# Kernel optimization log

Measured on AMD Instinct MI355X. Metric: run time of the kernel, lower is better.

## Reference

```python
import jax, jax.numpy as jnp
import numpy as np
from itertools import product

DEG = 3
N_COMPLEX = 8

def monomial_powers(deg: int, n_complex: int = 8) -> np.ndarray:
    out = [a for a in product(range(deg + 1), repeat=n_complex) if sum(a) <= deg]
    return np.asarray(out, dtype=np.int32)

POWERS = monomial_powers(DEG, N_COMPLEX)  # (K, 8)
K = POWERS.shape[0]                       # 165 for deg=3
MAXP = int(POWERS.max())                  # 3


def z_monomials(q):
    """q (B,16) real -> z^alpha (B,K) complex, z_k = q[:,k] + i q[:,k+8]."""
    x, y = q[:, :N_COMPLEX], q[:, N_COMPLEX:]
    z = jax.lax.complex(x, y)  # (B, 8)
    # power ladders z^0..z^MAXP : (B, 8, MAXP+1)
    cur = jnp.ones_like(z)
    ladders = [cur]
    for _ in range(MAXP):
        cur = cur * z
        ladders.append(cur)
    lad = jnp.stack(ladders, axis=-1)  # (B, 8, MAXP+1)
    mon = jnp.ones((q.shape[0], K), dtype=z.dtype)
    for c in range(N_COMPLEX):  # fixed 8 iterations (structural)
        mon = mon * lad[:, c, POWERS[:, c]]  # gather (B, K)
    return mon


def setup_inputs() -> dict:
    key = jax.random.key(0)
    kq, = jax.random.split(key, 1)
    B = 262144
    q = jax.random.normal(kq, (B, 16), dtype=jnp.float32)
    L_re = jnp.eye(K, dtype=jnp.float32)
    L_im = jnp.zeros((K, K), dtype=jnp.float32)
    return {"q": q, "L_re": L_re, "L_im": L_im}


def reference(q, L_re, L_im):
    # Cholesky-like factor L: strict lower triangles + softplus-positive diagonal
    Lr = jnp.tril(L_re, -1)
    Li = jnp.tril(L_im, -1)
    diag = jax.nn.softplus(jnp.diagonal(L_re)) + 0.001
    L = jax.lax.complex(Lr, Li) + jnp.diag(jax.lax.complex(diag, jnp.zeros_like(diag)))
    H = L @ L.conj().T                      # (K, K) Hermitian PSD
    z_a = z_monomials(q)                    # (B, K) complex64
    Hs = z_a @ H.T                          # (B, K)
    quad = jnp.sum(Hs * jnp.conj(z_a), axis=-1).real  # (B,)
    return jnp.log(quad + 1e-12)
```

## Files before the change

kernel.cpp:

```cpp
#include <hip/hip_runtime.h>
#include <hip/hip_bf16.h>
#include <utility>

#define DEV static __device__ __forceinline__

typedef __attribute__((ext_vector_type(8))) short bf16x8;
typedef __attribute__((ext_vector_type(4))) float f32x4;

constexpr int KM   = 165;
constexpr int IT   = 11;
constexpr int ITP  = 12;
constexpr int KS   = 6;
constexpr int NB   = ITP * KS * 64;
constexpr int ROWS = 64;

struct Pw { unsigned char p[8]; };
struct PwTab { Pw a[KM]; };
constexpr PwTab gen_powers() {
  PwTab t{};
  int idx = 0;
  for (int a0 = 0; a0 <= 3; ++a0)
  for (int a1 = 0; a1 <= 3-a0; ++a1)
  for (int a2 = 0; a2 <= 3-a0-a1; ++a2)
  for (int a3 = 0; a3 <= 3-a0-a1-a2; ++a3)
  for (int a4 = 0; a4 <= 3-a0-a1-a2-a3; ++a4)
  for (int a5 = 0; a5 <= 3-a0-a1-a2-a3-a4; ++a5)
  for (int a6 = 0; a6 <= 3-a0-a1-a2-a3-a4-a5; ++a6)
  for (int a7 = 0; a7 <= 3-a0-a1-a2-a3-a4-a5-a6; ++a7) {
    t.a[idx].p[0] = (unsigned char)a0; t.a[idx].p[1] = (unsigned char)a1;
    t.a[idx].p[2] = (unsigned char)a2; t.a[idx].p[3] = (unsigned char)a3;
    t.a[idx].p[4] = (unsigned char)a4; t.a[idx].p[5] = (unsigned char)a5;
    t.a[idx].p[6] = (unsigned char)a6; t.a[idx].p[7] = (unsigned char)a7;
    ++idx;
  }
  return t;
}
constexpr PwTab PW = gen_powers();

DEV unsigned int f2bf(float f) {
  unsigned int u = __builtin_bit_cast(unsigned int, f);
  u += 0x7fffu + ((u >> 16) & 1u);
  return u >> 16;
}
DEV unsigned int pack2(float lo, float hi) { return f2bf(lo) | (f2bf(hi) << 16); }
DEV float softplusf(float x) { return (x > 20.f) ? x : log1pf(expf(x)); }

template<int JJ, int C>
DEV void mono_step(float& r, float& i,
                   const float (&lx)[8][3], const float (&ly)[8][3]) {
  constexpr int pc = PW.a[JJ].p[C];
  if constexpr (pc > 0) {
    const float ar = lx[C][pc-1], ai = ly[C][pc-1];
    const float tr = r*ar - i*ai;
    i = r*ai + i*ar;
    r = tr;
  }
}
template<int JJ>
DEV void mono_eval(float& mr, float& mi,
                   const float (&lx)[8][3], const float (&ly)[8][3]) {
  float r = 1.f, i = 0.f;
  mono_step<JJ,0>(r,i,lx,ly); mono_step<JJ,1>(r,i,lx,ly);
  mono_step<JJ,2>(r,i,lx,ly); mono_step<JJ,3>(r,i,lx,ly);
  mono_step<JJ,4>(r,i,lx,ly); mono_step<JJ,5>(r,i,lx,ly);
  mono_step<JJ,6>(r,i,lx,ly); mono_step<JJ,7>(r,i,lx,ly);
  mr = r; mi = i;
}
template<int JJ>
DEV void mono_eval_guard(float& r, float& i,
                         const float (&lx)[8][3], const float (&ly)[8][3]) {
  if constexpr (JJ < KM) mono_eval<JJ>(r, i, lx, ly);
  else { r = 0.f; i = 0.f; }
}

template<int T, int... Us>
DEV void gen8(std::integer_sequence<int, Us...>, float (&mr)[8], float (&mi)[8],
              const float (&lx)[8][3], const float (&ly)[8][3]) {
  (mono_eval_guard<8*T + Us>(mr[Us], mi[Us], lx, ly), ...);
}
template<int T>
DEV void gen_chunk(const float (&lx)[8][3], const float (&ly)[8][3],
                   unsigned int* Xf, unsigned int* Yf, int mf, int r15) {
  constexpr int ksv = T >> 2;
  constexpr int gv  = T & 3;
  float mr[8], mi[8];
  gen8<T>(std::make_integer_sequence<int, 8>{}, mr, mi, lx, ly);
  uint4 ux, uy;
  ux.x = pack2(mr[0], mr[1]); ux.y = pack2(mr[2], mr[3]);
  ux.z = pack2(mr[4], mr[5]); ux.w = pack2(mr[6], mr[7]);
  uy.x = pack2(mi[0], mi[1]); uy.y = pack2(mi[2], mi[3]);
  uy.z = pack2(mi[4], mi[5]); uy.w = pack2(mi[6], mi[7]);
  const unsigned int off = (unsigned int)((mf*6 + ksv)*256 + gv*64 + r15*4);
  *(uint4*)&Xf[off] = ux;
  *(uint4*)&Yf[off] = uy;
}
template<int W, int... Ts>
DEV void gen_seq(std::integer_sequence<int, Ts...>,
                 const float (&lx)[8][3], const float (&ly)[8][3],
                 unsigned int* Xf, unsigned int* Yf, int mf, int r15) {
  (gen_chunk<6*W + Ts>(lx, ly, Xf, Yf, mf, r15), ...);
}
template<int W>
DEV void gen_wave(const float (&lx)[8][3], const float (&ly)[8][3],
                  unsigned int* Xf, unsigned int* Yf, int mf, int r15) {
  gen_seq<W>(std::make_integer_sequence<int, 6>{}, lx, ly, Xf, Yf, mf, r15);
}

__global__ void __launch_bounds__(256) poskahler_prep(
    const float* __restrict__ Lre, const float* __restrict__ Lim,
    uint4* __restrict__ bp, uint4* __restrict__ bq) {
  const int tid = blockIdx.x * 256 + threadIdx.x;
  if (tid >= NB) return;
  const int lane = tid & 63;
  const int it = (tid >> 6) / KS;
  const int ks = (tid >> 6) % KS;
  const int j  = it * 16 + (lane & 15);
  const int ib = ks * 32 + ((lane >> 4) << 3);
  float pr[8], qr[8];
#pragma unroll
  for (int e = 0; e < 8; ++e) { pr[e] = 0.f; qr[e] = 0.f; }
  if (j < KM) {
#pragma unroll
    for (int e = 0; e < 8; ++e) {
      const int i = ib + e;
      if (i < KM) {
        if (i > j)      { pr[e] = Lre[i*KM + j]; qr[e] = -Lim[i*KM + j]; }
        else if (i == j){ pr[e] = softplusf(Lre[j*KM + j]) + 0.001f; }
      }
    }
  }
  uint4 up, uq;
  up.x = pack2(pr[0], pr[1]); up.y = pack2(pr[2], pr[3]);
  up.z = pack2(pr[4], pr[5]); up.w = pack2(pr[6], pr[7]);
  uq.x = pack2(qr[0], qr[1]); uq.y = pack2(qr[2], qr[3]);
  uq.z = pack2(qr[4], qr[5]); uq.w = pack2(qr[6], qr[7]);
  bp[tid] = up;
  bq[tid] = uq;
}

template<int KSv>
DEV void load_tiles(const uint4* __restrict__ bp, const uint4* __restrict__ bq,
                    int wv, int lane, uint4 (&tp)[3], uint4 (&tq)[3]) {
#pragma unroll
  for (int ii = 0; ii < 3; ++ii) {
    const int it = 4*ii + wv;
    if (it <= 2*KSv + 1 && it < IT) {
      const int fs = (it*KS + KSv)*64 + lane;
      tp[ii] = bp[fs];
      tq[ii] = bq[fs];
    }
  }
}

template<int KSv>
DEV void compute_ks(const unsigned int* Xf, const unsigned int* Yf,
                    int wv, int lane,
                    const uint4 (&tp)[3], const uint4 (&tq)[3],
                    float (&aRe)[3][4][4], float (&aIm)[3][4][4]) {
  bf16x8 xf[4], yf[4];
#pragma unroll
  for (int mf = 0; mf < 4; ++mf) {
    const unsigned int off = (unsigned int)((mf*6 + KSv)*256 + lane*4);
    xf[mf] = __builtin_bit_cast(bf16x8, *(const uint4*)&Xf[off]);
    yf[mf] = __builtin_bit_cast(bf16x8, *(const uint4*)&Yf[off]);
  }
#pragma unroll
  for (int ii = 0; ii < 3; ++ii) {
    const int it = 4*ii + wv;
    if (it <= 2*KSv + 1 && it < IT) {
      const uint4 up = tp[ii];
      const uint4 uq = tq[ii];
      uint4 un;
      un.x = uq.x ^ 0x80008000u; un.y = uq.y ^ 0x80008000u;
      un.z = uq.z ^ 0x80008000u; un.w = uq.w ^ 0x80008000u;
      const bf16x8 vp = __builtin_bit_cast(bf16x8, up);
      const bf16x8 vq = __builtin_bit_cast(bf16x8, uq);
      const bf16x8 vn = __builtin_bit_cast(bf16x8, un);
#pragma unroll
      for (int mf = 0; mf < 4; ++mf) {
        f32x4 cre = { aRe[ii][mf][0], aRe[ii][mf][1], aRe[ii][mf][2], aRe[ii][mf][3] };
        f32x4 cim = { aIm[ii][mf][0], aIm[ii][mf][1], aIm[ii][mf][2], aIm[ii][mf][3] };
        cre = __builtin_amdgcn_mfma_f32_16x16x32_bf16(xf[mf], vp, cre, 0, 0, 0);
        cre = __builtin_amdgcn_mfma_f32_16x16x32_bf16(yf[mf], vq, cre, 0, 0, 0);
        cim = __builtin_amdgcn_mfma_f32_16x16x32_bf16(yf[mf], vp, cim, 0, 0, 0);
        cim = __builtin_amdgcn_mfma_f32_16x16x32_bf16(xf[mf], vn, cim, 0, 0, 0);
#pragma unroll
        for (int rr = 0; rr < 4; ++rr) { aRe[ii][mf][rr] = cre[rr]; aIm[ii][mf][rr] = cim[rr]; }
      }
    }
  }
}

__global__ void __launch_bounds__(256, 2) poskahler_main(
    const float* __restrict__ q,
    const uint4* __restrict__ bp, const uint4* __restrict__ bq,
    float* __restrict__ out) {
  __shared__ __align__(16) unsigned int Xf[6144];
  __shared__ __align__(16) unsigned int Yf[6144];
  __shared__ float qpart[4][ROWS];

  const int t     = threadIdx.x;
  const int lane  = t & 63;
  const int wv    = t >> 6;
  const int bbase = blockIdx.x * ROWS;
  const int mf_r  = lane >> 4;
  const int r15   = lane & 15;

  uint4 tpA[3] = {}, tqA[3] = {}, tpB[3] = {}, tqB[3] = {};
  load_tiles<0>(bp, bq, wv, lane, tpA, tqA);
  load_tiles<1>(bp, bq, wv, lane, tpB, tqB);

  {
    const float* qr = q + (size_t)(bbase + lane) * 16;
    const float4 q0 = ((const float4*)qr)[0];
    const float4 q1 = ((const float4*)qr)[1];
    const float4 q2 = ((const float4*)qr)[2];
    const float4 q3 = ((const float4*)qr)[3];
    const float xs[8] = {q0.x,q0.y,q0.z,q0.w,q1.x,q1.y,q1.z,q1.w};
    const float ys[8] = {q2.x,q2.y,q2.z,q2.w,q3.x,q3.y,q3.z,q3.w};
    float lx[8][3], ly[8][3];
#pragma unroll
    for (int c = 0; c < 8; ++c) {
      const float xr = xs[c], yi = ys[c];
      lx[c][0] = xr;             ly[c][0] = yi;
      lx[c][1] = xr*xr - yi*yi;  ly[c][1] = 2.f*xr*yi;
      lx[c][2] = lx[c][1]*xr - ly[c][1]*yi;
      ly[c][2] = lx[c][1]*yi + ly[c][1]*xr;
    }
    switch (wv) {
      case 0: gen_wave<0>(lx, ly, Xf, Yf, mf_r, r15); break;
      case 1: gen_wave<1>(lx, ly, Xf, Yf, mf_r, r15); break;
      case 2: gen_wave<2>(lx, ly, Xf, Yf, mf_r, r15); break;
      default: gen_wave<3>(lx, ly, Xf, Yf, mf_r, r15); break;
    }
  }
  __syncthreads();

  float aRe[3][4][4], aIm[3][4][4];
#pragma unroll
  for (int ii = 0; ii < 3; ++ii)
#pragma unroll
    for (int mf = 0; mf < 4; ++mf)
#pragma unroll
      for (int rr = 0; rr < 4; ++rr) { aRe[ii][mf][rr] = 0.f; aIm[ii][mf][rr] = 0.f; }

  compute_ks<0>(Xf, Yf, wv, lane, tpA, tqA, aRe, aIm);
  load_tiles<2>(bp, bq, wv, lane, tpA, tqA);
  compute_ks<1>(Xf, Yf, wv, lane, tpB, tqB, aRe, aIm);
  load_tiles<3>(bp, bq, wv, lane, tpB, tqB);
  compute_ks<2>(Xf, Yf, wv, lane, tpA, tqA, aRe, aIm);
  load_tiles<4>(bp, bq, wv, lane, tpA, tqA);
  compute_ks<3>(Xf, Yf, wv, lane, tpB, tqB, aRe, aIm);
  load_tiles<5>(bp, bq, wv, lane, tpB, tqB);
  compute_ks<4>(Xf, Yf, wv, lane, tpA, tqA, aRe, aIm);
  compute_ks<5>(Xf, Yf, wv, lane, tpB, tqB, aRe, aIm);

  float p[4][4];
#pragma unroll
  for (int mf = 0; mf < 4; ++mf)
#pragma unroll
    for (int rr = 0; rr < 4; ++rr) p[mf][rr] = 0.f;

#pragma unroll
  for (int ii = 0; ii < 3; ++ii)
#pragma unroll
    for (int mf = 0; mf < 4; ++mf)
#pragma unroll
      for (int rr = 0; rr < 4; ++rr)
        p[mf][rr] += aRe[ii][mf][rr]*aRe[ii][mf][rr] + aIm[ii][mf][rr]*aIm[ii][mf][rr];

#pragma unroll
  for (int mf = 0; mf < 4; ++mf)
#pragma unroll
    for (int rr = 0; rr < 4; ++rr) {
      float v = p[mf][rr];
      v += __shfl_xor(v, 1);
      v += __shfl_xor(v, 2);
      v += __shfl_xor(v, 4);
      v += __shfl_xor(v, 8);
      p[mf][rr] = v;
    }

  if (r15 == 0) {
#pragma unroll
    for (int mf = 0; mf < 4; ++mf)
#pragma unroll
      for (int rr = 0; rr < 4; ++rr)
        qpart[wv][mf*16 + 4*(lane >> 4) + rr] = p[mf][rr];
  }
  __syncthreads();
  if (t < ROWS) {
    const float quad = qpart[0][t] + qpart[1][t] + qpart[2][t] + qpart[3][t];
    out[bbase + t] = logf(quad + 1e-12f);
  }
}

extern "C" void kernel_launch(void* const* d_in, const int* in_sizes, int n_in,
                              void* d_out, int out_size, void* d_ws, size_t ws_size,
                              hipStream_t stream) {
  const float* q   = (const float*)d_in[0];
  const float* Lre = (const float*)d_in[1];
  const float* Lim = (const float*)d_in[2];
  float* out = (float*)d_out;
  uint4* bp = (uint4*)d_ws;
  uint4* bq = bp + NB;
  const int B = in_sizes[0] / 16;
  poskahler_prep<<<(NB + 255)/256, 256, 0, stream>>>(Lre, Lim, bp, bq);
  poskahler_main<<<B / ROWS, 256, 0, stream>>>(q, bp, bq, out);
}
```

Measured before the change: 56.85 us.

## Split each block's GEMM across eight waves by row-fragment pairs

```diff
diff --git a/kernel.cpp b/kernel.cpp
--- a/kernel.cpp
+++ b/kernel.cpp
@@ -94,16 +94,12 @@
   *(uint4*)&Xf[off] = ux;
   *(uint4*)&Yf[off] = uy;
 }
-template<int W, int... Ts>
-DEV void gen_seq(std::integer_sequence<int, Ts...>,
-                 const float (&lx)[8][3], const float (&ly)[8][3],
-                 unsigned int* Xf, unsigned int* Yf, int mf, int r15) {
-  (gen_chunk<6*W + Ts>(lx, ly, Xf, Yf, mf, r15), ...);
-}
 template<int W>
 DEV void gen_wave(const float (&lx)[8][3], const float (&ly)[8][3],
                   unsigned int* Xf, unsigned int* Yf, int mf, int r15) {
-  gen_seq<W>(std::make_integer_sequence<int, 6>{}, lx, ly, Xf, Yf, mf, r15);
+  gen_chunk<3*W+0>(lx, ly, Xf, Yf, mf, r15);
+  gen_chunk<3*W+1>(lx, ly, Xf, Yf, mf, r15);
+  gen_chunk<3*W+2>(lx, ly, Xf, Yf, mf, r15);
 }
 
 __global__ void __launch_bounds__(256) poskahler_prep(
@@ -140,10 +136,10 @@
 
 template<int KSv>
 DEV void load_tiles(const uint4* __restrict__ bp, const uint4* __restrict__ bq,
-                    int wv, int lane, uint4 (&tp)[3], uint4 (&tq)[3]) {
+                    int itb, int lane, uint4 (&tp)[3], uint4 (&tq)[3]) {
 #pragma unroll
   for (int ii = 0; ii < 3; ++ii) {
-    const int it = 4*ii + wv;
+    const int it = 4*ii + itb;
     if (it <= 2*KSv + 1 && it < IT) {
       const int fs = (it*KS + KSv)*64 + lane;
       tp[ii] = bp[fs];
@@ -154,61 +150,61 @@
 
 template<int KSv>
 DEV void compute_ks(const unsigned int* Xf, const unsigned int* Yf,
-                    int wv, int lane,
+                    int itb, int mfp, int lane,
                     const uint4 (&tp)[3], const uint4 (&tq)[3],
-                    float (&aRe)[3][4][4], float (&aIm)[3][4][4]) {
-  bf16x8 xf[4], yf[4];
-#pragma unroll
-  for (int mf = 0; mf < 4; ++mf) {
-    const unsigned int off = (unsigned int)((mf*6 + KSv)*256 + lane*4);
-    xf[mf] = __builtin_bit_cast(bf16x8, *(const uint4*)&Xf[off]);
-    yf[mf] = __builtin_bit_cast(bf16x8, *(const uint4*)&Yf[off]);
-  }
-#pragma unroll
-  for (int ii = 0; ii < 3; ++ii) {
-    const int it = 4*ii + wv;
-    if (it <= 2*KSv + 1 && it < IT) {
-      const uint4 up = tp[ii];
-      const uint4 uq = tq[ii];
-      uint4 un;
-      un.x = uq.x ^ 0x80008000u; un.y = uq.y ^ 0x80008000u;
-      un.z = uq.z ^ 0x80008000u; un.w = uq.w ^ 0x80008000u;
-      const bf16x8 vp = __builtin_bit_cast(bf16x8, up);
-      const bf16x8 vq = __builtin_bit_cast(bf16x8, uq);
-      const bf16x8 vn = __builtin_bit_cast(bf16x8, un);
-#pragma unroll
-      for (int mf = 0; mf < 4; ++mf) {
-        f32x4 cre = { aRe[ii][mf][0], aRe[ii][mf][1], aRe[ii][mf][2], aRe[ii][mf][3] };
-        f32x4 cim = { aIm[ii][mf][0], aIm[ii][mf][1], aIm[ii][mf][2], aIm[ii][mf][3] };
-        cre = __builtin_amdgcn_mfma_f32_16x16x32_bf16(xf[mf], vp, cre, 0, 0, 0);
-        cre = __builtin_amdgcn_mfma_f32_16x16x32_bf16(yf[mf], vq, cre, 0, 0, 0);
-        cim = __builtin_amdgcn_mfma_f32_16x16x32_bf16(yf[mf], vp, cim, 0, 0, 0);
-        cim = __builtin_amdgcn_mfma_f32_16x16x32_bf16(xf[mf], vn, cim, 0, 0, 0);
-#pragma unroll
-        for (int rr = 0; rr < 4; ++rr) { aRe[ii][mf][rr] = cre[rr]; aIm[ii][mf][rr] = cim[rr]; }
+                    float (&aRe)[3][2][4], float (&aIm)[3][2][4]) {
+  if (itb > 2*KSv + 1) return;
+#pragma unroll
+  for (int m2 = 0; m2 < 2; ++m2) {
+    const int mf = 2*mfp + m2;
+    const unsigned int off = (unsigned int)((mf*6 + KSv)*256) + (unsigned int)lane*4;
+    const bf16x8 xf = __builtin_bit_cast(bf16x8, *(const uint4*)&Xf[off]);
+    const bf16x8 yf = __builtin_bit_cast(bf16x8, *(const uint4*)&Yf[off]);
+#pragma unroll
+    for (int ii = 0; ii < 3; ++ii) {
+      const int it = 4*ii + itb;
+      if (it <= 2*KSv + 1 && it < IT) {
+        const uint4 up = tp[ii];
+        const uint4 uq = tq[ii];
+        uint4 un;
+        un.x = uq.x ^ 0x80008000u; un.y = uq.y ^ 0x80008000u;
+        un.z = uq.z ^ 0x80008000u; un.w = uq.w ^ 0x80008000u;
+        const bf16x8 vp = __builtin_bit_cast(bf16x8, up);
+        const bf16x8 vq = __builtin_bit_cast(bf16x8, uq);
+        const bf16x8 vn = __builtin_bit_cast(bf16x8, un);
+        f32x4 cre = { aRe[ii][m2][0], aRe[ii][m2][1], aRe[ii][m2][2], aRe[ii][m2][3] };
+        f32x4 cim = { aIm[ii][m2][0], aIm[ii][m2][1], aIm[ii][m2][2], aIm[ii][m2][3] };
+        cre = __builtin_amdgcn_mfma_f32_16x16x32_bf16(xf, vp, cre, 0, 0, 0);
+        cre = __builtin_amdgcn_mfma_f32_16x16x32_bf16(yf, vq, cre, 0, 0, 0);
+        cim = __builtin_amdgcn_mfma_f32_16x16x32_bf16(yf, vp, cim, 0, 0, 0);
+        cim = __builtin_amdgcn_mfma_f32_16x16x32_bf16(xf, vn, cim, 0, 0, 0);
+#pragma unroll
+        for (int rr = 0; rr < 4; ++rr) { aRe[ii][m2][rr] = cre[rr]; aIm[ii][m2][rr] = cim[rr]; }
       }
     }
   }
 }
 
-__global__ void __launch_bounds__(256, 2) poskahler_main(
+__global__ void __launch_bounds__(512, 4) poskahler_main(
     const float* __restrict__ q,
     const uint4* __restrict__ bp, const uint4* __restrict__ bq,
     float* __restrict__ out) {
   __shared__ __align__(16) unsigned int Xf[6144];
   __shared__ __align__(16) unsigned int Yf[6144];
-  __shared__ float qpart[4][ROWS];
+  __shared__ float qpart[8][ROWS];
 
   const int t     = threadIdx.x;
   const int lane  = t & 63;
   const int wv    = t >> 6;
+  const int itb   = wv & 3;
+  const int mfp   = wv >> 2;
   const int bbase = blockIdx.x * ROWS;
   const int mf_r  = lane >> 4;
   const int r15   = lane & 15;
 
   uint4 tpA[3] = {}, tqA[3] = {}, tpB[3] = {}, tqB[3] = {};
-  load_tiles<0>(bp, bq, wv, lane, tpA, tqA);
-  load_tiles<1>(bp, bq, wv, lane, tpB, tqB);
+  load_tiles<0>(bp, bq, itb, lane, tpA, tqA);
+  load_tiles<1>(bp, bq, itb, lane, tpB, tqB);
 
   {
     const float* qr = q + (size_t)(bbase + lane) * 16;
@@ -231,66 +227,72 @@
       case 0: gen_wave<0>(lx, ly, Xf, Yf, mf_r, r15); break;
       case 1: gen_wave<1>(lx, ly, Xf, Yf, mf_r, r15); break;
       case 2: gen_wave<2>(lx, ly, Xf, Yf, mf_r, r15); break;
-      default: gen_wave<3>(lx, ly, Xf, Yf, mf_r, r15); break;
+      case 3: gen_wave<3>(lx, ly, Xf, Yf, mf_r, r15); break;
+      case 4: gen_wave<4>(lx, ly, Xf, Yf, mf_r, r15); break;
+      case 5: gen_wave<5>(lx, ly, Xf, Yf, mf_r, r15); break;
+      case 6: gen_wave<6>(lx, ly, Xf, Yf, mf_r, r15); break;
+      default:gen_wave<7>(lx, ly, Xf, Yf, mf_r, r15); break;
     }
   }
   __syncthreads();
 
-  float aRe[3][4][4], aIm[3][4][4];
+  float aRe[3][2][4], aIm[3][2][4];
 #pragma unroll
   for (int ii = 0; ii < 3; ++ii)
 #pragma unroll
-    for (int mf = 0; mf < 4; ++mf)
-#pragma unroll
-      for (int rr = 0; rr < 4; ++rr) { aRe[ii][mf][rr] = 0.f; aIm[ii][mf][rr] = 0.f; }
-
-  compute_ks<0>(Xf, Yf, wv, lane, tpA, tqA, aRe, aIm);
-  load_tiles<2>(bp, bq, wv, lane, tpA, tqA);
-  compute_ks<1>(Xf, Yf, wv, lane, tpB, tqB, aRe, aIm);
-  load_tiles<3>(bp, bq, wv, lane, tpB, tqB);
-  compute_ks<2>(Xf, Yf, wv, lane, tpA, tqA, aRe, aIm);
-  load_tiles<4>(bp, bq, wv, lane, tpA, tqA);
-  compute_ks<3>(Xf, Yf, wv, lane, tpB, tqB, aRe, aIm);
-  load_tiles<5>(bp, bq, wv, lane, tpB, tqB);
-  compute_ks<4>(Xf, Yf, wv, lane, tpA, tqA, aRe, aIm);
-  compute_ks<5>(Xf, Yf, wv, lane, tpB, tqB, aRe, aIm);
-
-  float p[4][4];
-#pragma unroll
-  for (int mf = 0; mf < 4; ++mf)
-#pragma unroll
-    for (int rr = 0; rr < 4; ++rr) p[mf][rr] = 0.f;
+    for (int m2 = 0; m2 < 2; ++m2)
+#pragma unroll
+      for (int rr = 0; rr < 4; ++rr) { aRe[ii][m2][rr] = 0.f; aIm[ii][m2][rr] = 0.f; }
+
+  compute_ks<0>(Xf, Yf, itb, mfp, lane, tpA, tqA, aRe, aIm);
+  load_tiles<2>(bp, bq, itb, lane, tpA, tqA);
+  compute_ks<1>(Xf, Yf, itb, mfp, lane, tpB, tqB, aRe, aIm);
+  load_tiles<3>(bp, bq, itb, lane, tpB, tqB);
+  compute_ks<2>(Xf, Yf, itb, mfp, lane, tpA, tqA, aRe, aIm);
+  load_tiles<4>(bp, bq, itb, lane, tpA, tqA);
+  compute_ks<3>(Xf, Yf, itb, mfp, lane, tpB, tqB, aRe, aIm);
+  load_tiles<5>(bp, bq, itb, lane, tpB, tqB);
+  compute_ks<4>(Xf, Yf, itb, mfp, lane, tpA, tqA, aRe, aIm);
+  compute_ks<5>(Xf, Yf, itb, mfp, lane, tpB, tqB, aRe, aIm);
+
+  float p[2][4];
+#pragma unroll
+  for (int m2 = 0; m2 < 2; ++m2)
+#pragma unroll
+    for (int rr = 0; rr < 4; ++rr) p[m2][rr] = 0.f;
 
 #pragma unroll
   for (int ii = 0; ii < 3; ++ii)
 #pragma unroll
-    for (int mf = 0; mf < 4; ++mf)
+    for (int m2 = 0; m2 < 2; ++m2)
 #pragma unroll
       for (int rr = 0; rr < 4; ++rr)
-        p[mf][rr] += aRe[ii][mf][rr]*aRe[ii][mf][rr] + aIm[ii][mf][rr]*aIm[ii][mf][rr];
-
-#pragma unroll
-  for (int mf = 0; mf < 4; ++mf)
+        p[m2][rr] += aRe[ii][m2][rr]*aRe[ii][m2][rr] + aIm[ii][m2][rr]*aIm[ii][m2][rr];
+
+#pragma unroll
+  for (int m2 = 0; m2 < 2; ++m2)
 #pragma unroll
     for (int rr = 0; rr < 4; ++rr) {
-      float v = p[mf][rr];
+      float v = p[m2][rr];
       v += __shfl_xor(v, 1);
       v += __shfl_xor(v, 2);
       v += __shfl_xor(v, 4);
       v += __shfl_xor(v, 8);
-      p[mf][rr] = v;
+      p[m2][rr] = v;
     }
 
   if (r15 == 0) {
-#pragma unroll
-    for (int mf = 0; mf < 4; ++mf)
+    const int g = lane >> 4;
+#pragma unroll
+    for (int m2 = 0; m2 < 2; ++m2)
 #pragma unroll
       for (int rr = 0; rr < 4; ++rr)
-        qpart[wv][mf*16 + 4*(lane >> 4) + rr] = p[mf][rr];
+        qpart[wv][(2*mfp + m2)*16 + 4*g + rr] = p[m2][rr];
   }
   __syncthreads();
   if (t < ROWS) {
-    const float quad = qpart[0][t] + qpart[1][t] + qpart[2][t] + qpart[3][t];
+    const int pb = 4 * (t >> 5);
+    const float quad = qpart[pb][t] + qpart[pb+1][t] + qpart[pb+2][t] + qpart[pb+3][t];
     out[bbase + t] = logf(quad + 1e-12f);
   }
 }
@@ -306,5 +308,5 @@
   uint4* bq = bp + NB;
   const int B = in_sizes[0] / 16;
   poskahler_prep<<<(NB + 255)/256, 256, 0, stream>>>(Lre, Lim, bp, bq);
-  poskahler_main<<<B / ROWS, 256, 0, stream>>>(q, bp, bq, out);
-}
+  poskahler_main<<<B / ROWS, 512, 0, stream>>>(q, bp, bq, out);
+}
```

Measured after the change: 65.10 us. +14.5%, slower.

## Warp-specialize main kernel into persistent producer/consumer waves with double-buffered LDS

Applied to the files above, without the earlier changes.

```diff
diff --git a/kernel.cpp b/kernel.cpp
--- a/kernel.cpp
+++ b/kernel.cpp
@@ -106,6 +106,32 @@
   gen_seq<W>(std::make_integer_sequence<int, 6>{}, lx, ly, Xf, Yf, mf, r15);
 }
 
+DEV void gen_rowset(const float* __restrict__ q, int rs, int lane, int gw,
+                    unsigned int* Xb, unsigned int* Yb, int mf_r, int r15) {
+  const float* qr = q + ((size_t)rs * ROWS + lane) * 16;
+  const float4 q0 = ((const float4*)qr)[0];
+  const float4 q1 = ((const float4*)qr)[1];
+  const float4 q2 = ((const float4*)qr)[2];
+  const float4 q3 = ((const float4*)qr)[3];
+  const float xs[8] = {q0.x,q0.y,q0.z,q0.w,q1.x,q1.y,q1.z,q1.w};
+  const float ys[8] = {q2.x,q2.y,q2.z,q2.w,q3.x,q3.y,q3.z,q3.w};
+  float lx[8][3], ly[8][3];
+#pragma unroll
+  for (int c = 0; c < 8; ++c) {
+    const float xr = xs[c], yi = ys[c];
+    lx[c][0] = xr;             ly[c][0] = yi;
+    lx[c][1] = xr*xr - yi*yi;  ly[c][1] = 2.f*xr*yi;
+    lx[c][2] = lx[c][1]*xr - ly[c][1]*yi;
+    ly[c][2] = lx[c][1]*yi + ly[c][1]*xr;
+  }
+  switch (gw) {
+    case 0: gen_wave<0>(lx, ly, Xb, Yb, mf_r, r15); break;
+    case 1: gen_wave<1>(lx, ly, Xb, Yb, mf_r, r15); break;
+    case 2: gen_wave<2>(lx, ly, Xb, Yb, mf_r, r15); break;
+    default: gen_wave<3>(lx, ly, Xb, Yb, mf_r, r15); break;
+  }
+}
+
 __global__ void __launch_bounds__(256) poskahler_prep(
     const float* __restrict__ Lre, const float* __restrict__ Lim,
     uint4* __restrict__ bp, uint4* __restrict__ bq) {
@@ -157,10 +183,11 @@
                     int wv, int lane,
                     const uint4 (&tp)[3], const uint4 (&tq)[3],
                     float (&aRe)[3][4][4], float (&aIm)[3][4][4]) {
+  if (wv > 2*KSv + 1) return;
   bf16x8 xf[4], yf[4];
 #pragma unroll
   for (int mf = 0; mf < 4; ++mf) {
-    const unsigned int off = (unsigned int)((mf*6 + KSv)*256 + lane*4);
+    const unsigned int off = (unsigned int)((mf*6 + KSv)*256) + (unsigned int)lane*4;
     xf[mf] = __builtin_bit_cast(bf16x8, *(const uint4*)&Xf[off]);
     yf[mf] = __builtin_bit_cast(bf16x8, *(const uint4*)&Yf[off]);
   }
@@ -191,107 +218,111 @@
   }
 }
 
-__global__ void __launch_bounds__(256, 2) poskahler_main(
+__global__ void __launch_bounds__(512, 2) poskahler_main(
     const float* __restrict__ q,
     const uint4* __restrict__ bp, const uint4* __restrict__ bq,
-    float* __restrict__ out) {
-  __shared__ __align__(16) unsigned int Xf[6144];
-  __shared__ __align__(16) unsigned int Yf[6144];
-  __shared__ float qpart[4][ROWS];
+    float* __restrict__ out, int nrs) {
+  __shared__ __align__(16) unsigned int Xls[2*6144];
+  __shared__ __align__(16) unsigned int Yls[2*6144];
+  __shared__ float qp[2][4][ROWS];
 
   const int t     = threadIdx.x;
   const int lane  = t & 63;
-  const int wv    = t >> 6;
-  const int bbase = blockIdx.x * ROWS;
+  const int wv8   = t >> 6;
+  const bool genw = (wv8 >= 4);
+  const int wv    = wv8 & 3;
   const int mf_r  = lane >> 4;
   const int r15   = lane & 15;
+  const int gstr  = gridDim.x;
 
   uint4 tpA[3] = {}, tqA[3] = {}, tpB[3] = {}, tqB[3] = {};
-  load_tiles<0>(bp, bq, wv, lane, tpA, tqA);
-  load_tiles<1>(bp, bq, wv, lane, tpB, tqB);
-
-  {
-    const float* qr = q + (size_t)(bbase + lane) * 16;
-    const float4 q0 = ((const float4*)qr)[0];
-    const float4 q1 = ((const float4*)qr)[1];
-    const float4 q2 = ((const float4*)qr)[2];
-    const float4 q3 = ((const float4*)qr)[3];
-    const float xs[8] = {q0.x,q0.y,q0.z,q0.w,q1.x,q1.y,q1.z,q1.w};
-    const float ys[8] = {q2.x,q2.y,q2.z,q2.w,q3.x,q3.y,q3.z,q3.w};
-    float lx[8][3], ly[8][3];
-#pragma unroll
-    for (int c = 0; c < 8; ++c) {
-      const float xr = xs[c], yi = ys[c];
-      lx[c][0] = xr;             ly[c][0] = yi;
-      lx[c][1] = xr*xr - yi*yi;  ly[c][1] = 2.f*xr*yi;
-      lx[c][2] = lx[c][1]*xr - ly[c][1]*yi;
-      ly[c][2] = lx[c][1]*yi + ly[c][1]*xr;
+  int r = blockIdx.x;
+  int i = 0;
+
+  if (genw) {
+    gen_rowset(q, r, lane, wv, Xls, Yls, mf_r, r15);
+  } else {
+    load_tiles<0>(bp, bq, wv, lane, tpA, tqA);
+    load_tiles<1>(bp, bq, wv, lane, tpB, tqB);
+  }
+
+  while (true) {
+    __syncthreads();
+    const int par = i & 1;
+    if (!genw) {
+      const unsigned int* Xb = Xls + par*6144;
+      const unsigned int* Yb = Yls + par*6144;
+      float aRe[3][4][4], aIm[3][4][4];
+#pragma unroll
+      for (int ii = 0; ii < 3; ++ii)
+#pragma unroll
+        for (int mf = 0; mf < 4; ++mf)
+#pragma unroll
+          for (int rr = 0; rr < 4; ++rr) { aRe[ii][mf][rr] = 0.f; aIm[ii][mf][rr] = 0.f; }
+
+      compute_ks<0>(Xb, Yb, wv, lane, tpA, tqA, aRe, aIm);
+      load_tiles<2>(bp, bq, wv, lane, tpA, tqA);
+      compute_ks<1>(Xb, Yb, wv, lane, tpB, tqB, aRe, aIm);
+      load_tiles<3>(bp, bq, wv, lane, tpB, tqB);
+      compute_ks<2>(Xb, Yb, wv, lane, tpA, tqA, aRe, aIm);
+      load_tiles<4>(bp, bq, wv, lane, tpA, tqA);
+      compute_ks<3>(Xb, Yb, wv, lane, tpB, tqB, aRe, aIm);
+      load_tiles<5>(bp, bq, wv, lane, tpB, tqB);
+      compute_ks<4>(Xb, Yb, wv, lane, tpA, tqA, aRe, aIm);
+      load_tiles<0>(bp, bq, wv, lane, tpA, tqA);
+      compute_ks<5>(Xb, Yb, wv, lane, tpB, tqB, aRe, aIm);
+      load_tiles<1>(bp, bq, wv, lane, tpB, tqB);
+
+      float p[4][4];
+#pragma unroll
+      for (int mf = 0; mf < 4; ++mf)
+#pragma unroll
+        for (int rr = 0; rr < 4; ++rr) p[mf][rr] = 0.f;
+#pragma unroll
+      for (int ii = 0; ii < 3; ++ii)
+#pragma unroll
+        for (int mf = 0; mf < 4; ++mf)
+#pragma unroll
+          for (int rr = 0; rr < 4; ++rr)
+            p[mf][rr] += aRe[ii][mf][rr]*aRe[ii][mf][rr] + aIm[ii][mf][rr]*aIm[ii][mf][rr];
+#pragma unroll
+      for (int mf = 0; mf < 4; ++mf)
+#pragma unroll
+        for (int rr = 0; rr < 4; ++rr) {
+          float v = p[mf][rr];
+          v += __shfl_xor(v, 1);
+          v += __shfl_xor(v, 2);
+          v += __shfl_xor(v, 4);
+          v += __shfl_xor(v, 8);
+          p[mf][rr] = v;
+        }
+      if (r15 == 0) {
+        const int g = lane >> 4;
+#pragma unroll
+        for (int mf = 0; mf < 4; ++mf)
+#pragma unroll
+          for (int rr = 0; rr < 4; ++rr)
+            qp[par][wv][mf*16 + 4*g + rr] = p[mf][rr];
+      }
+    } else {
+      if (wv == 0 && i >= 1) {
+        const float quad = qp[1-par][0][lane] + qp[1-par][1][lane]
+                         + qp[1-par][2][lane] + qp[1-par][3][lane];
+        out[(size_t)(r - gstr) * ROWS + lane] = logf(quad + 1e-12f);
+      }
+      if (r + gstr < nrs)
+        gen_rowset(q, r + gstr, lane, wv, Xls + (1-par)*6144, Yls + (1-par)*6144, mf_r, r15);
     }
-    switch (wv) {
-      case 0: gen_wave<0>(lx, ly, Xf, Yf, mf_r, r15); break;
-      case 1: gen_wave<1>(lx, ly, Xf, Yf, mf_r, r15); break;
-      case 2: gen_wave<2>(lx, ly, Xf, Yf, mf_r, r15); break;
-      default: gen_wave<3>(lx, ly, Xf, Yf, mf_r, r15); break;
-    }
-  }
+    if (r + gstr >= nrs) break;
+    ++i; r += gstr;
+  }
+
   __syncthreads();
-
-  float aRe[3][4][4], aIm[3][4][4];
-#pragma unroll
-  for (int ii = 0; ii < 3; ++ii)
-#pragma unroll
-    for (int mf = 0; mf < 4; ++mf)
-#pragma unroll
-      for (int rr = 0; rr < 4; ++rr) { aRe[ii][mf][rr] = 0.f; aIm[ii][mf][rr] = 0.f; }
-
-  compute_ks<0>(Xf, Yf, wv, lane, tpA, tqA, aRe, aIm);
-  load_tiles<2>(bp, bq, wv, lane, tpA, tqA);
-  compute_ks<1>(Xf, Yf, wv, lane, tpB, tqB, aRe, aIm);
-  load_tiles<3>(bp, bq, wv, lane, tpB, tqB);
-  compute_ks<2>(Xf, Yf, wv, lane, tpA, tqA, aRe, aIm);
-  load_tiles<4>(bp, bq, wv, lane, tpA, tqA);
-  compute_ks<3>(Xf, Yf, wv, lane, tpB, tqB, aRe, aIm);
-  load_tiles<5>(bp, bq, wv, lane, tpB, tqB);
-  compute_ks<4>(Xf, Yf, wv, lane, tpA, tqA, aRe, aIm);
-  compute_ks<5>(Xf, Yf, wv, lane, tpB, tqB, aRe, aIm);
-
-  float p[4][4];
-#pragma unroll
-  for (int mf = 0; mf < 4; ++mf)
-#pragma unroll
-    for (int rr = 0; rr < 4; ++rr) p[mf][rr] = 0.f;
-
-#pragma unroll
-  for (int ii = 0; ii < 3; ++ii)
-#pragma unroll
-    for (int mf = 0; mf < 4; ++mf)
-#pragma unroll
-      for (int rr = 0; rr < 4; ++rr)
-        p[mf][rr] += aRe[ii][mf][rr]*aRe[ii][mf][rr] + aIm[ii][mf][rr]*aIm[ii][mf][rr];
-
-#pragma unroll
-  for (int mf = 0; mf < 4; ++mf)
-#pragma unroll
-    for (int rr = 0; rr < 4; ++rr) {
-      float v = p[mf][rr];
-      v += __shfl_xor(v, 1);
-      v += __shfl_xor(v, 2);
-      v += __shfl_xor(v, 4);
-      v += __shfl_xor(v, 8);
-      p[mf][rr] = v;
-    }
-
-  if (r15 == 0) {
-#pragma unroll
-    for (int mf = 0; mf < 4; ++mf)
-#pragma unroll
-      for (int rr = 0; rr < 4; ++rr)
-        qpart[wv][mf*16 + 4*(lane >> 4) + rr] = p[mf][rr];
-  }
-  __syncthreads();
-  if (t < ROWS) {
-    const float quad = qpart[0][t] + qpart[1][t] + qpart[2][t] + qpart[3][t];
-    out[bbase + t] = logf(quad + 1e-12f);
+  if (genw && wv == 0) {
+    const int par = i & 1;
+    const float quad = qp[par][0][lane] + qp[par][1][lane]
+                     + qp[par][2][lane] + qp[par][3][lane];
+    out[(size_t)r * ROWS + lane] = logf(quad + 1e-12f);
   }
 }
 
@@ -305,6 +336,7 @@
   uint4* bp = (uint4*)d_ws;
   uint4* bq = bp + NB;
   const int B = in_sizes[0] / 16;
+  const int nrs = B / ROWS;
   poskahler_prep<<<(NB + 255)/256, 256, 0, stream>>>(Lre, Lim, bp, bq);
-  poskahler_main<<<B / ROWS, 256, 0, stream>>>(q, bp, bq, out);
-}
+  poskahler_main<<<256, 512, 0, stream>>>(q, bp, bq, out, nrs);
+}
```

Result: slower. 65.25 us (+14.8%).
